# Kernel optimization log

Measured on AMD Instinct MI355X. Metric: run time of the kernel, lower is better.

## Reference

```python
import math
import jax, jax.numpy as jnp
import numpy as np

B, T, C, HS = 4, 4096, 2048, 128

def setup_inputs() -> dict:
    key = jax.random.key(0)
    k1, k2, k3, k4 = jax.random.split(key, 4)
    x = jax.random.normal(k1, (B, T, C), dtype=jnp.float32)
    # torch Linear init ~ U(-1/sqrt(in), 1/sqrt(in)); normal*0.02 is fine for a numeric baseline
    Wq = jax.random.normal(k2, (C, HS), dtype=jnp.float32) * 0.02
    Wk = jax.random.normal(k3, (C, HS), dtype=jnp.float32) * 0.02
    Wv = jax.random.normal(k4, (C, HS), dtype=jnp.float32) * 0.02
    return {"x": x, "Wq": Wq, "Wk": Wk, "Wv": Wv}

def reference(x, Wq, Wk, Wv):
    # Single-head causal self-attention (dropout in eval mode = identity).
    q = x @ Wq          # [B,T,HS]
    k = x @ Wk          # [B,T,HS]
    v = x @ Wv          # [B,T,HS]
    scale = 1.0 / math.sqrt(HS)
    att = jnp.einsum('bqd,bkd->bqk', q, k) * scale          # [B,T,T]
    causal = jnp.tril(jnp.ones((T, T), dtype=bool))          # [T,T]
    att = jnp.where(causal[None, :, :], att, -jnp.inf)
    att = jax.nn.softmax(att, axis=-1)
    y = jnp.einsum('bqk,bkd->bqd', att, v)                   # [B,T,HS]
    return y
```

## Files before the change

kernel.cpp:

```cpp
#include <hip/hip_runtime.h>
#include <hip/hip_bf16.h>


#define B_  4
#define T_  4096
#define C_  2048
#define HS_ 128

typedef unsigned short u16;
typedef __attribute__((ext_vector_type(8))) short short8;
typedef __attribute__((ext_vector_type(4))) float floatx4;

static __device__ __forceinline__ u16 f2bf(float x) {
  union { float f; unsigned u; } c; c.f = x;
  unsigned r = 0x7fffu + ((c.u >> 16) & 1u);
  return (u16)((c.u + r) >> 16);
}
static __device__ __forceinline__ u16 cvt_elem(float x) { return f2bf(x); }
static __device__ __forceinline__ u16 cvt_elem(u16 x) { return x; }

template <typename ST>
__global__ __launch_bounds__(256) void transpose_kernel(
    const ST* __restrict__ src, u16* __restrict__ dst, int R, int C) {
  __shared__ u16 tile[32][33];
  size_t moff = (size_t)blockIdx.z * (size_t)R * (size_t)C;
  src += moff; dst += moff;
  int c0 = blockIdx.x * 32, r0 = blockIdx.y * 32;
  int tx = threadIdx.x, ty = threadIdx.y;
#pragma unroll
  for (int i = 0; i < 4; ++i)
    tile[ty + 8 * i][tx] = cvt_elem(src[(size_t)(r0 + ty + 8 * i) * C + (c0 + tx)]);
  __syncthreads();
#pragma unroll
  for (int i = 0; i < 4; ++i)
    dst[(size_t)(c0 + ty + 8 * i) * R + (r0 + tx)] = tile[tx][ty + 8 * i];
}

#define GBM 128
#define GBK 64
#define LPAD 72

__global__ __launch_bounds__(256) void qkv_gemm_kernel(
    const float* __restrict__ X, const u16* __restrict__ WT3,
    u16* __restrict__ qkv) {
  __shared__ u16 Xs[GBM][LPAD];
  __shared__ u16 Ws[HS_][LPAD];
  int z = blockIdx.y;
  const u16* Wt = WT3 + (size_t)z * HS_ * C_;
  u16* outp = qkv + (size_t)z * ((size_t)B_ * T_ * HS_);
  int t = threadIdx.x;
  int wv = t >> 6, lane = t & 63;
  int l15 = lane & 15, hi = lane >> 4;
  int wm = (wv & 1) * 64, wn = (wv >> 1) * 64;
  size_t mbase = (size_t)blockIdx.x * GBM;

  floatx4 acc[4][4];
#pragma unroll
  for (int i = 0; i < 4; ++i)
#pragma unroll
    for (int j = 0; j < 4; ++j) acc[i][j] = (floatx4){0.f, 0.f, 0.f, 0.f};

  for (int kt = 0; kt < C_ / GBK; ++kt) {
#pragma unroll
    for (int i = 0; i < 4; ++i) {
      int id = i * 256 + t;
      int m = id >> 3, c = id & 7;
      const float* sp = &X[(mbase + m) * C_ + kt * GBK + c * 8];
      short8 v;
#pragma unroll
      for (int j = 0; j < 8; ++j) v[j] = (short)f2bf(sp[j]);
      *(short8*)&Xs[m][c * 8] = v;
    }
#pragma unroll
    for (int i = 0; i < 4; ++i) {
      int id = i * 256 + t;
      int n = id >> 3, c = id & 7;
      *(short8*)&Ws[n][c * 8] =
          *(const short8*)&Wt[(size_t)n * C_ + kt * GBK + c * 8];
    }
    __syncthreads();
#pragma unroll
    for (int ks = 0; ks < 2; ++ks) {
      short8 af[4], bf[4];
#pragma unroll
      for (int mt = 0; mt < 4; ++mt)
        af[mt] = *(const short8*)&Xs[wm + mt * 16 + l15][ks * 32 + hi * 8];
#pragma unroll
      for (int nt = 0; nt < 4; ++nt)
        bf[nt] = *(const short8*)&Ws[wn + nt * 16 + l15][ks * 32 + hi * 8];
#pragma unroll
      for (int mt = 0; mt < 4; ++mt)
#pragma unroll
        for (int nt = 0; nt < 4; ++nt)
          acc[mt][nt] = __builtin_amdgcn_mfma_f32_16x16x32_bf16(
              af[mt], bf[nt], acc[mt][nt], 0, 0, 0);
    }
    __syncthreads();
  }
#pragma unroll
  for (int mt = 0; mt < 4; ++mt)
#pragma unroll
    for (int nt = 0; nt < 4; ++nt)
#pragma unroll
      for (int r = 0; r < 4; ++r) {
        size_t row = mbase + wm + mt * 16 + hi * 4 + r;
        int col = wn + nt * 16 + l15;
        outp[row * HS_ + col] = f2bf(acc[mt][nt][r]);
      }
}

#define BQ 64
#define BKV 64

__global__ __launch_bounds__(256) void flash_attn_kernel(
    const u16* __restrict__ q, const u16* __restrict__ k,
    const u16* __restrict__ vT, float* __restrict__ out) {
  __shared__ u16 Ks[BKV][136];
  __shared__ u16 Vs[HS_][72];
  __shared__ u16 Ps[BQ][72];
  int b = blockIdx.y, qb = blockIdx.x;
  int t = threadIdx.x;
  int wv = t >> 6, lane = t & 63, l15 = lane & 15, hi = lane >> 4;

  const float sc = 0.08838834764831845f * 1.4426950408889634f;

  short8 qf[4];
  {
    const u16* qrow = q + (size_t)(b * T_ + qb * BQ + wv * 16 + l15) * HS_;
#pragma unroll
    for (int ks = 0; ks < 4; ++ks)
      qf[ks] = *(const short8*)(qrow + ks * 32 + hi * 8);
  }

  floatx4 of[8];
#pragma unroll
  for (int dt = 0; dt < 8; ++dt) of[dt] = (floatx4){0.f, 0.f, 0.f, 0.f};
  float m_run[4], l_run[4];
#pragma unroll
  for (int r = 0; r < 4; ++r) { m_run[r] = -__builtin_inff(); l_run[r] = 0.f; }

  const u16* kbase = k + (size_t)b * T_ * HS_;
  const u16* vbase = vT + (size_t)b * HS_ * T_;

  for (int kb = 0; kb <= qb; ++kb) {
#pragma unroll
    for (int i = 0; i < 4; ++i) {
      int id = i * 256 + t;
      int n = id >> 4, c = id & 15;
      *(short8*)&Ks[n][c * 8] =
          *(const short8*)&kbase[(size_t)(kb * BKV + n) * HS_ + c * 8];
    }
#pragma unroll
    for (int i = 0; i < 4; ++i) {
      int id = i * 256 + t;
      int d = id >> 3, c = id & 7;
      *(short8*)&Vs[d][c * 8] =
          *(const short8*)&vbase[(size_t)d * T_ + kb * BKV + c * 8];
    }
    __syncthreads();

    floatx4 sf[4];
#pragma unroll
    for (int nt = 0; nt < 4; ++nt) {
      floatx4 s = (floatx4){0.f, 0.f, 0.f, 0.f};
#pragma unroll
      for (int ks = 0; ks < 4; ++ks) {
        short8 bfrag = *(const short8*)&Ks[nt * 16 + l15][ks * 32 + hi * 8];
        s = __builtin_amdgcn_mfma_f32_16x16x32_bf16(qf[ks], bfrag, s, 0, 0, 0);
      }
      sf[nt] = s;
    }

    float sv[4][4];
    if (kb == qb) {
#pragma unroll
      for (int nt = 0; nt < 4; ++nt) {
        int col = nt * 16 + l15;
#pragma unroll
        for (int r = 0; r < 4; ++r) {
          int row = wv * 16 + hi * 4 + r;
          sv[nt][r] = (col <= row) ? sf[nt][r] * sc : -__builtin_inff();
        }
      }
    } else {
#pragma unroll
      for (int nt = 0; nt < 4; ++nt)
#pragma unroll
        for (int r = 0; r < 4; ++r) sv[nt][r] = sf[nt][r] * sc;
    }

    float mt4[4], alpha[4];
#pragma unroll
    for (int r = 0; r < 4; ++r)
      mt4[r] = fmaxf(fmaxf(sv[0][r], sv[1][r]), fmaxf(sv[2][r], sv[3][r]));
#pragma unroll
    for (int off = 1; off < 16; off <<= 1)
#pragma unroll
      for (int r = 0; r < 4; ++r)
        mt4[r] = fmaxf(mt4[r], __shfl_xor(mt4[r], off));
#pragma unroll
    for (int r = 0; r < 4; ++r) {
      float mn = fmaxf(m_run[r], mt4[r]);
      alpha[r] = exp2f(m_run[r] - mn);
      m_run[r] = mn;
    }
    float pv[4][4], lt[4];
#pragma unroll
    for (int nt = 0; nt < 4; ++nt)
#pragma unroll
      for (int r = 0; r < 4; ++r) pv[nt][r] = exp2f(sv[nt][r] - m_run[r]);
#pragma unroll
    for (int r = 0; r < 4; ++r)
      lt[r] = (pv[0][r] + pv[1][r]) + (pv[2][r] + pv[3][r]);
#pragma unroll
    for (int off = 1; off < 16; off <<= 1)
#pragma unroll
      for (int r = 0; r < 4; ++r) lt[r] += __shfl_xor(lt[r], off);
#pragma unroll
    for (int r = 0; r < 4; ++r) l_run[r] = l_run[r] * alpha[r] + lt[r];
#pragma unroll
    for (int dt = 0; dt < 8; ++dt)
#pragma unroll
      for (int r = 0; r < 4; ++r) of[dt][r] *= alpha[r];

#pragma unroll
    for (int nt = 0; nt < 4; ++nt)
#pragma unroll
      for (int r = 0; r < 4; ++r)
        Ps[wv * 16 + hi * 4 + r][nt * 16 + l15] = f2bf(pv[nt][r]);
    __asm__ volatile("s_waitcnt lgkmcnt(0)" ::: "memory");

#pragma unroll
    for (int ks2 = 0; ks2 < 2; ++ks2) {
      short8 af = *(const short8*)&Ps[wv * 16 + l15][ks2 * 32 + hi * 8];
#pragma unroll
      for (int dt = 0; dt < 8; ++dt) {
        short8 bfrag = *(const short8*)&Vs[dt * 16 + l15][ks2 * 32 + hi * 8];
        of[dt] = __builtin_amdgcn_mfma_f32_16x16x32_bf16(af, bfrag, of[dt], 0, 0, 0);
      }
    }
    __syncthreads();
  }

  float rl[4];
#pragma unroll
  for (int r = 0; r < 4; ++r) rl[r] = 1.0f / l_run[r];
#pragma unroll
  for (int dt = 0; dt < 8; ++dt)
#pragma unroll
    for (int r = 0; r < 4; ++r) {
      size_t row = (size_t)(b * T_ + qb * BQ + wv * 16 + hi * 4 + r);
      out[row * HS_ + dt * 16 + l15] = of[dt][r] * rl[r];
    }
}

extern "C" void kernel_launch(void* const* d_in, const int* in_sizes, int n_in,
                              void* d_out, int out_size, void* d_ws, size_t ws_size,
                              hipStream_t stream) {
  const float* x  = (const float*)d_in[0];
  const float* Wq = (const float*)d_in[1];
  const float* Wk = (const float*)d_in[2];
  const float* Wv = (const float*)d_in[3];
  float* out = (float*)d_out;

  u16* ws = (u16*)d_ws;
  const size_t wtsz  = (size_t)HS_ * C_;
  const size_t qkvsz = (size_t)B_ * T_ * HS_;
  u16* WT = ws;
  u16* qv = WT + 3 * wtsz;
  u16* kv = qv + qkvsz;
  u16* vv = kv + qkvsz;
  u16* vT = vv + qkvsz;

  dim3 tb(32, 8);
  transpose_kernel<float><<<dim3(HS_ / 32, C_ / 32, 1), tb, 0, stream>>>(Wq, WT + 0 * wtsz, C_, HS_);
  transpose_kernel<float><<<dim3(HS_ / 32, C_ / 32, 1), tb, 0, stream>>>(Wk, WT + 1 * wtsz, C_, HS_);
  transpose_kernel<float><<<dim3(HS_ / 32, C_ / 32, 1), tb, 0, stream>>>(Wv, WT + 2 * wtsz, C_, HS_);

  qkv_gemm_kernel<<<dim3((B_ * T_) / GBM, 3), 256, 0, stream>>>(x, WT, qv);

  transpose_kernel<u16><<<dim3(HS_ / 32, T_ / 32, B_), tb, 0, stream>>>(vv, vT, T_, HS_);

  flash_attn_kernel<<<dim3(T_ / BQ, B_), 256, 0, stream>>>(qv, kv, vT, out);
}
```

Measured before the change: 375.7 us.

## Split causal attention across KV chunks with a separate merge kernel

Splits each query block's causal KV range into chunks of 16 blocks that run as independent workgroups. Each workgroup writes unnormalized partial outputs plus running max and sum. A merge kernel then combines them with log-sum-exp weights. This targets load imbalance and low occupancy from the triangular causal work, at the cost of extra workspace traffic and a second launch. It falls back to the original kernel when the workspace is too small.

```diff
diff --git a/kernel.cpp b/kernel.cpp
--- a/kernel.cpp
+++ b/kernel.cpp
@@ -111,14 +111,17 @@
 
 #define BQ 64
 #define BKV 64
-
-__global__ __launch_bounds__(256) void flash_attn_kernel(
+#define CHUNK 16
+
+template <bool WRITE_PARTIAL>
+static __device__ __forceinline__ void flash_body(
     const u16* __restrict__ q, const u16* __restrict__ k,
-    const u16* __restrict__ vT, float* __restrict__ out) {
+    const u16* __restrict__ vT, float* __restrict__ outO,
+    float* __restrict__ Mp, float* __restrict__ Lp,
+    int b, int qb, int kb0, int kb1, int slot) {
   __shared__ u16 Ks[BKV][136];
   __shared__ u16 Vs[HS_][72];
   __shared__ u16 Ps[BQ][72];
-  int b = blockIdx.y, qb = blockIdx.x;
   int t = threadIdx.x;
   int wv = t >> 6, lane = t & 63, l15 = lane & 15, hi = lane >> 4;
 
@@ -142,7 +145,7 @@
   const u16* kbase = k + (size_t)b * T_ * HS_;
   const u16* vbase = vT + (size_t)b * HS_ * T_;
 
-  for (int kb = 0; kb <= qb; ++kb) {
+  for (int kb = kb0; kb <= kb1; ++kb) {
 #pragma unroll
     for (int i = 0; i < 4; ++i) {
       int id = i * 256 + t;
@@ -242,16 +245,92 @@
     __syncthreads();
   }
 
-  float rl[4];
-#pragma unroll
-  for (int r = 0; r < 4; ++r) rl[r] = 1.0f / l_run[r];
-#pragma unroll
-  for (int dt = 0; dt < 8; ++dt)
-#pragma unroll
-    for (int r = 0; r < 4; ++r) {
-      size_t row = (size_t)(b * T_ + qb * BQ + wv * 16 + hi * 4 + r);
-      out[row * HS_ + dt * 16 + l15] = of[dt][r] * rl[r];
-    }
+  if (WRITE_PARTIAL) {
+    float* Op = outO + (size_t)slot * (BQ * HS_);
+#pragma unroll
+    for (int dt = 0; dt < 8; ++dt)
+#pragma unroll
+      for (int r = 0; r < 4; ++r) {
+        int row = wv * 16 + hi * 4 + r;
+        Op[row * HS_ + dt * 16 + l15] = of[dt][r];
+      }
+    if (l15 == 0) {
+#pragma unroll
+      for (int r = 0; r < 4; ++r) {
+        int row = wv * 16 + hi * 4 + r;
+        Mp[slot * BQ + row] = m_run[r];
+        Lp[slot * BQ + row] = l_run[r];
+      }
+    }
+  } else {
+    float rl[4];
+#pragma unroll
+    for (int r = 0; r < 4; ++r) rl[r] = 1.0f / l_run[r];
+#pragma unroll
+    for (int dt = 0; dt < 8; ++dt)
+#pragma unroll
+      for (int r = 0; r < 4; ++r) {
+        size_t row = (size_t)(b * T_ + qb * BQ + wv * 16 + hi * 4 + r);
+        outO[row * HS_ + dt * 16 + l15] = of[dt][r] * rl[r];
+      }
+  }
+}
+
+__global__ __launch_bounds__(256) void flash_partial_kernel(
+    const u16* __restrict__ q, const u16* __restrict__ k,
+    const u16* __restrict__ vT, float* __restrict__ Opart,
+    float* __restrict__ Mpart, float* __restrict__ Lpart) {
+  int qb = blockIdx.x, c = blockIdx.y, b = blockIdx.z;
+  int kb0 = c * CHUNK;
+  if (kb0 > qb) return;
+  int kb1 = min(qb, kb0 + CHUNK - 1);
+  int slot = (b * (T_ / BQ) + qb) * 4 + c;
+  flash_body<true>(q, k, vT, Opart, Mpart, Lpart, b, qb, kb0, kb1, slot);
+}
+
+__global__ __launch_bounds__(256) void flash_attn_kernel(
+    const u16* __restrict__ q, const u16* __restrict__ k,
+    const u16* __restrict__ vT, float* __restrict__ out) {
+  int qb = blockIdx.x, b = blockIdx.y;
+  flash_body<false>(q, k, vT, out, nullptr, nullptr, b, qb, 0, qb, 0);
+}
+
+__global__ __launch_bounds__(256) void flash_merge_kernel(
+    const float* __restrict__ Opart, const float* __restrict__ Mpart,
+    const float* __restrict__ Lpart, float* __restrict__ out) {
+  __shared__ float w[4][BQ];
+  __shared__ float invL[BQ];
+  int qb = blockIdx.x, b = blockIdx.y;
+  int t = threadIdx.x;
+  int nch = qb / CHUNK + 1;
+  int slot0 = (b * (T_ / BQ) + qb) * 4;
+
+  if (t < BQ) {
+    float mv[4], mmax = -__builtin_inff();
+    for (int c = 0; c < nch; ++c) {
+      mv[c] = Mpart[(slot0 + c) * BQ + t];
+      mmax = fmaxf(mmax, mv[c]);
+    }
+    float L = 0.f;
+    for (int c = 0; c < nch; ++c) {
+      float wc = exp2f(mv[c] - mmax);
+      w[c][t] = wc;
+      L += wc * Lpart[(slot0 + c) * BQ + t];
+    }
+    invL[t] = 1.0f / L;
+  }
+  __syncthreads();
+
+  size_t obase = ((size_t)(b * T_) + (size_t)qb * BQ) * HS_;
+#pragma unroll
+  for (int j = 0; j < 32; ++j) {
+    int e = j * 256 + t;
+    int row = e >> 7;
+    float acc = 0.f;
+    for (int c = 0; c < nch; ++c)
+      acc += w[c][row] * Opart[(size_t)(slot0 + c) * (BQ * HS_) + e];
+    out[obase + e] = acc * invL[row];
+  }
 }
 
 extern "C" void kernel_launch(void* const* d_in, const int* in_sizes, int n_in,
@@ -271,6 +350,14 @@
   u16* kv = qv + qkvsz;
   u16* vv = kv + qkvsz;
   u16* vT = vv + qkvsz;
+  const size_t base_bytes = (3 * wtsz + 4 * qkvsz) * sizeof(u16);
+
+  const int NSLOT = B_ * (T_ / BQ) * 4;
+  float* Opart = (float*)((char*)d_ws + base_bytes);
+  float* Mpart = Opart + (size_t)NSLOT * BQ * HS_;
+  float* Lpart = Mpart + (size_t)NSLOT * BQ;
+  const size_t split_bytes =
+      base_bytes + ((size_t)NSLOT * BQ * HS_ + 2 * (size_t)NSLOT * BQ) * sizeof(float);
 
   dim3 tb(32, 8);
   transpose_kernel<float><<<dim3(HS_ / 32, C_ / 32, 1), tb, 0, stream>>>(Wq, WT + 0 * wtsz, C_, HS_);
@@ -281,5 +368,12 @@
 
   transpose_kernel<u16><<<dim3(HS_ / 32, T_ / 32, B_), tb, 0, stream>>>(vv, vT, T_, HS_);
 
-  flash_attn_kernel<<<dim3(T_ / BQ, B_), 256, 0, stream>>>(qv, kv, vT, out);
-}
+  if (ws_size >= split_bytes) {
+    flash_partial_kernel<<<dim3(T_ / BQ, 4, B_), 256, 0, stream>>>(
+        qv, kv, vT, Opart, Mpart, Lpart);
+    flash_merge_kernel<<<dim3(T_ / BQ, B_), 256, 0, stream>>>(
+        Opart, Mpart, Lpart, out);
+  } else {
+    flash_attn_kernel<<<dim3(T_ / BQ, B_), 256, 0, stream>>>(qv, kv, vT, out);
+  }
+}
```

Result: faster. 352.3 us (-6.2%).
